# Performance work log

Hardware: AMD Instinct MI355X
Metric: run time of the kernel (lower is better)

The kernel has to match this reference:

```python
import jax, jax.numpy as jnp
import numpy as np

DIM = 1024
NUM_HEADS = 16
SEQ_LEN = 4096


def setup_inputs() -> dict:
    key = jax.random.key(0)
    ks = jax.random.split(key, 9)
    s = DIM ** -0.5  # typical init scale for weights
    return {
        "x": jax.random.normal(ks[0], (SEQ_LEN, DIM), dtype=jnp.float32),
        "Wq": jax.random.normal(ks[1], (DIM, DIM), dtype=jnp.float32) * s,
        "bq": jax.random.normal(ks[2], (DIM,), dtype=jnp.float32) * s,
        "Wk": jax.random.normal(ks[3], (DIM, DIM), dtype=jnp.float32) * s,
        "bk": jax.random.normal(ks[4], (DIM,), dtype=jnp.float32) * s,
        "Wv": jax.random.normal(ks[5], (DIM, DIM), dtype=jnp.float32) * s,
        "bv": jax.random.normal(ks[6], (DIM,), dtype=jnp.float32) * s,
        "Wp": jax.random.normal(ks[7], (DIM, DIM), dtype=jnp.float32) * s,
        "bp": jax.random.normal(ks[8], (DIM,), dtype=jnp.float32) * s,
    }


def reference(x, Wq, bq, Wk, bk, Wv, bv, Wp, bp):
    T, C = x.shape
    H = NUM_HEADS
    Dh = C // H
    # QKV projections (eqx.nn.Linear: y = W @ x + b, vmapped over tokens)
    q = (x @ Wq.T + bq).reshape(T, H, Dh).swapaxes(0, 1)  # [H, T, Dh]
    k = (x @ Wk.T + bk).reshape(T, H, Dh).swapaxes(0, 1)
    v = (x @ Wv.T + bv).reshape(T, H, Dh).swapaxes(0, 1)
    # NOTE: original scales by C**-0.5 (full dim), not head_dim**-0.5
    attn = jnp.einsum("htd,hsd->hts", q, k) * (C ** -0.5)  # [H, T, T]
    causal = jnp.tril(jnp.ones((T, T), dtype=bool))[None, :, :]
    attn = jnp.where(causal, attn, -jnp.inf)
    attn = jax.nn.softmax(attn, axis=-1)
    out = jnp.einsum("hts,hsd->htd", attn, v)  # [H, T, Dh]
    out = out.swapaxes(0, 1).reshape(T, C)
    return out @ Wp.T + bp
```

## Files before the change

### kernel.cpp

```cpp
#include <hip/hip_runtime.h>
#include <stdint.h>

typedef unsigned short u16;
typedef __bf16 bf16x8 __attribute__((ext_vector_type(8)));
typedef u16 u16x8 __attribute__((ext_vector_type(8)));
typedef u16 u16x4 __attribute__((ext_vector_type(4)));
typedef float f32x4 __attribute__((ext_vector_type(4)));
typedef float f32x16 __attribute__((ext_vector_type(16)));

#define SEQ 4096
#define CD 1024
#define NH 16
#define DHD 64

__device__ __forceinline__ u16 f2bf(float f) {
  union { float f; unsigned u; } v; v.f = f;
  unsigned r = v.u + 0x7fffu + ((v.u >> 16) & 1u);
  return (u16)(r >> 16);
}
__device__ __forceinline__ unsigned fbits(float f) {
  union { float f; unsigned u; } v; v.f = f; return v.u;
}

__device__ __forceinline__ void load_lds16(const u16* g, u16* l) {
  __builtin_amdgcn_global_load_lds((const __attribute__((address_space(1))) void*)g,
                                   (__attribute__((address_space(3))) void*)l, 16, 0, 0);
}

__global__ __launch_bounds__(256) void cvt_all(const float* __restrict__ x, const float* __restrict__ Wq,
                                               const float* __restrict__ Wk, const float* __restrict__ Wv,
                                               const float* __restrict__ Wp,
                                               u16* __restrict__ xb, u16* __restrict__ Wb, u16* __restrict__ Wpb) {
  int b = blockIdx.x;
  const float* src; u16* dst; int base;
  if (b < 2048)      { src = x;  dst = xb;             base = b; }
  else if (b < 2560) { src = Wq; dst = Wb;             base = b - 2048; }
  else if (b < 3072) { src = Wk; dst = Wb + CD * CD;   base = b - 2560; }
  else if (b < 3584) { src = Wv; dst = Wb + 2*CD*CD;   base = b - 3072; }
  else               { src = Wp; dst = Wpb;            base = b - 3584; }
  int i = (base * 256 + (int)threadIdx.x) * 8;
  float4 a = *(const float4*)(src + i);
  float4 c = *(const float4*)(src + i + 4);
  u16x8 o;
  o[0] = f2bf(a.x); o[1] = f2bf(a.y); o[2] = f2bf(a.z); o[3] = f2bf(a.w);
  o[4] = f2bf(c.x); o[5] = f2bf(c.y); o[6] = f2bf(c.z); o[7] = f2bf(c.w);
  *(u16x8*)(dst + i) = o;
}

template<int MODE>
__device__ __forceinline__ void gemm_core(const u16* __restrict__ A, const u16* __restrict__ Bw,
                                          const float* __restrict__ bias, void* __restrict__ outp,
                                          float oscale) {
  constexpr int K = CD, N = CD;
  __shared__ u16 As[128 * 32];
  __shared__ u16 Bs[128 * 32];
  const int tid = threadIdx.x;
  const int w = tid >> 6, L = tid & 63, q = L >> 4, ln = L & 15;
  const int rowA0 = blockIdx.y * 128, rowB0 = blockIdx.x * 128;
  const int wr = (w >> 1) * 64, wc = (w & 1) * 64;
  f32x4 acc[4][4] = {};
  for (int k0 = 0; k0 < K; k0 += 32) {
#pragma unroll
    for (int pass = 0; pass < 2; ++pass) {
      int off = pass * 4096 + tid * 16;
      int row = off >> 6;
      int cole = (off & 63) >> 1;
      load_lds16(A + (size_t)(rowA0 + row) * K + k0 + cole, As + pass * 2048 + w * 512);
      load_lds16(Bw + (size_t)(rowB0 + row) * K + k0 + cole, Bs + pass * 2048 + w * 512);
    }
    __syncthreads();
    bf16x8 af[4], bg[4];
#pragma unroll
    for (int i = 0; i < 4; ++i) af[i] = *(const bf16x8*)(As + (wr + i * 16 + ln) * 32 + q * 8);
#pragma unroll
    for (int i = 0; i < 4; ++i) bg[i] = *(const bf16x8*)(Bs + (wc + i * 16 + ln) * 32 + q * 8);
#pragma unroll
    for (int i = 0; i < 4; ++i)
#pragma unroll
      for (int j = 0; j < 4; ++j)
        acc[i][j] = __builtin_amdgcn_mfma_f32_16x16x32_bf16(af[i], bg[j], acc[i][j], 0, 0, 0);
    __syncthreads();
  }
#pragma unroll
  for (int i = 0; i < 4; ++i) {
#pragma unroll
    for (int j = 0; j < 4; ++j) {
      int col = rowB0 + wc + j * 16 + ln;
      float bb = bias[col];
#pragma unroll
      for (int r = 0; r < 4; ++r) {
        int row = rowA0 + wr + i * 16 + q * 4 + r;
        float v = (acc[i][j][r] + bb) * oscale;
        if (MODE == 0)      ((u16*)outp)[(size_t)row * N + col] = f2bf(v);
        else if (MODE == 1) ((u16*)outp)[(size_t)col * SEQ + row] = f2bf(v);
        else                ((float*)outp)[(size_t)row * N + col] = v;
      }
    }
  }
}

__global__ __launch_bounds__(256) void gemm_qkv(const u16* __restrict__ A, const u16* __restrict__ W3,
                                                const float* __restrict__ bq, const float* __restrict__ bk,
                                                const float* __restrict__ bv, u16* __restrict__ Qb,
                                                u16* __restrict__ Kb, u16* __restrict__ VTb) {
  int z = blockIdx.z;
  if (z == 0)      gemm_core<0>(A, W3,               bq, Qb,  0.03125f);
  else if (z == 1) gemm_core<0>(A, W3 + CD * CD,     bk, Kb,  1.0f);
  else             gemm_core<1>(A, W3 + 2 * CD * CD, bv, VTb, 1.0f);
}

__global__ __launch_bounds__(256) void gemm_proj(const u16* __restrict__ A, const u16* __restrict__ Bw,
                                                 const float* __restrict__ bias, float* __restrict__ out) {
  gemm_core<2>(A, Bw, bias, out, 1.0f);
}

__global__ __launch_bounds__(128) void attn_kernel(const u16* __restrict__ Q, const u16* __restrict__ Kg,
                                                   const u16* __restrict__ VTg, u16* __restrict__ O) {
  __shared__ u16 Ks[2][64 * 72];
  __shared__ u16 Vt[2][64 * 72];
  const int tid = threadIdx.x, w = tid >> 6, L = tid & 63;
  const int ln = L & 31, hh = L >> 5;
  const int b = blockIdx.x;
  const int qt = (SEQ / 64 - 1) - (b >> 4);
  const int h = b & 15;
  const int colH = h * DHD;
  const int qrow0 = qt * 64 + w * 32;
  bf16x8 qf[4];
#pragma unroll
  for (int kk = 0; kk < 4; ++kk)
    qf[kk] = *(const bf16x8*)(Q + (size_t)(qrow0 + ln) * CD + colH + kk * 16 + hh * 8);
  f32x16 oa[2] = {};
  float lsum = 0.f;
  const int srow = tid >> 3, sx = tid & 7;
  u16x8 kr[4], vr[4];
#pragma unroll
  for (int p = 0; p < 4; ++p) {
    kr[p] = *(const u16x8*)(Kg + (size_t)(p * 16 + srow) * CD + colH + sx * 8);
    vr[p] = *(const u16x8*)(VTg + (size_t)(colH + p * 16 + srow) * SEQ + sx * 8);
  }
  for (int jt = 0; jt <= qt; ++jt) {
    const int buf = jt & 1;
    u16* KsB = Ks[buf];
    u16* VtB = Vt[buf];
#pragma unroll
    for (int p = 0; p < 4; ++p) {
      *(u16x8*)(KsB + (p * 16 + srow) * 72 + sx * 8) = kr[p];
      *(u16x8*)(VtB + (p * 16 + srow) * 72 + sx * 8) = vr[p];
    }
    __syncthreads();
    if (jt < qt) {
      const size_t kb2 = (size_t)(jt + 1) * 64;
#pragma unroll
      for (int p = 0; p < 4; ++p) {
        kr[p] = *(const u16x8*)(Kg + (kb2 + p * 16 + srow) * CD + colH + sx * 8);
        vr[p] = *(const u16x8*)(VTg + (size_t)(colH + p * 16 + srow) * SEQ + kb2 + sx * 8);
      }
    }
    const bool diag = (jt == qt);
    unsigned pk[16];
#pragma unroll
    for (int nt = 0; nt < 2; ++nt) {
      f32x16 a = {};
#pragma unroll
      for (int kk = 0; kk < 4; ++kk) {
        bf16x8 kf = *(const bf16x8*)(KsB + (nt * 32 + ln) * 72 + kk * 16 + hh * 8);
        a = __builtin_amdgcn_mfma_f32_32x32x16_bf16(kf, qf[kk], a, 0, 0, 0);
      }
#pragma unroll
      for (int r = 0; r < 16; ++r) {
        float sv = a[r];
        if (diag) {
          const int key_l = nt * 32 + (r & 3) + 8 * (r >> 2) + 4 * hh;
          if (key_l > w * 32 + ln) sv = -1e30f;
        }
        float p = __expf(sv);
        lsum += p;
        a[r] = p;
      }
#pragma unroll
      for (int i = 0; i < 8; ++i)
        pk[nt * 8 + i] = __builtin_amdgcn_perm(fbits(a[2 * i + 1]), fbits(a[2 * i]), 0x07060302);
    }
#pragma unroll
    for (int b0 = 0; b0 < 16; b0 += 4) {
      asm("v_permlane32_swap_b32 %0, %1" : "+v"(pk[b0 + 0]), "+v"(pk[b0 + 2]));
      asm("v_permlane32_swap_b32 %0, %1" : "+v"(pk[b0 + 1]), "+v"(pk[b0 + 3]));
    }
#pragma unroll
    for (int g = 0; g < 2; ++g)
#pragma unroll
      for (int s = 0; s < 4; ++s) {
        bf16x8 vf = *(const bf16x8*)(VtB + (g * 32 + ln) * 72 + s * 16 + hh * 8);
        union { unsigned u[4]; bf16x8 v; } pf;
        pf.u[0] = pk[s * 4 + 0]; pf.u[1] = pk[s * 4 + 1];
        pf.u[2] = pk[s * 4 + 2]; pf.u[3] = pk[s * 4 + 3];
        oa[g] = __builtin_amdgcn_mfma_f32_32x32x16_bf16(vf, pf.v, oa[g], 0, 0, 0);
      }
  }
  lsum += __shfl_xor(lsum, 32, 64);
  const float inv = 1.0f / lsum;
#pragma unroll
  for (int g = 0; g < 2; ++g)
#pragma unroll
    for (int rg = 0; rg < 4; ++rg) {
      u16x4 ov;
#pragma unroll
      for (int i = 0; i < 4; ++i) ov[i] = f2bf(oa[g][rg * 4 + i] * inv);
      *(u16x4*)(O + (size_t)(qrow0 + ln) * CD + colH + g * 32 + 8 * rg + 4 * hh) = ov;
    }
}

extern "C" void kernel_launch(void* const* d_in, const int* in_sizes, int n_in,
                              void* d_out, int out_size, void* d_ws, size_t ws_size,
                              hipStream_t stream) {
  const float* x  = (const float*)d_in[0];
  const float* Wq = (const float*)d_in[1];
  const float* bq = (const float*)d_in[2];
  const float* Wk = (const float*)d_in[3];
  const float* bk = (const float*)d_in[4];
  const float* Wv = (const float*)d_in[5];
  const float* bv = (const float*)d_in[6];
  const float* Wp = (const float*)d_in[7];
  const float* bp = (const float*)d_in[8];

  char* ws = (char*)d_ws;
  u16* xb  = (u16*)(ws);
  u16* Wb  = (u16*)(ws + (8u << 20));
  u16* Wpb = (u16*)(ws + (14u << 20));
  u16* Qb  = (u16*)(ws + (16u << 20));
  u16* Kb  = (u16*)(ws + (24u << 20));
  u16* VTb = (u16*)(ws + (32u << 20));
  u16* Ab  = (u16*)(ws + (40u << 20));

  cvt_all<<<4096, 256, 0, stream>>>(x, Wq, Wk, Wv, Wp, xb, Wb, Wpb);
  gemm_qkv<<<dim3(CD / 128, SEQ / 128, 3), 256, 0, stream>>>(xb, Wb, bq, bk, bv, Qb, Kb, VTb);
  attn_kernel<<<(SEQ / 64) * NH, 128, 0, stream>>>(Qb, Kb, VTb, Ab);
  gemm_proj<<<dim3(CD / 128, SEQ / 128), 256, 0, stream>>>(Ab, Wpb, bp, (float*)d_out);
}
```

Baseline: 222.7 us.

## Double-buffer GEMM LDS tiles with register prefetch; split conversion kernel

Replaces the direct global-to-LDS loads in the shared GEMM core with register prefetch of the next K tile into a double-buffered LDS array. This drops one barrier per iteration and overlaps global loads with MFMA work. It also splits the single fused fp32-to-bf16 conversion kernel into five separate launches. The split adds launch overhead, and routing tiles through registers raises register pressure and adds LDS write instructions.

```diff
diff --git a/kernel.cpp b/kernel.cpp
--- a/kernel.cpp
+++ b/kernel.cpp
@@ -22,29 +22,15 @@
   union { float f; unsigned u; } v; v.f = f; return v.u;
 }
 
-__device__ __forceinline__ void load_lds16(const u16* g, u16* l) {
-  __builtin_amdgcn_global_load_lds((const __attribute__((address_space(1))) void*)g,
-                                   (__attribute__((address_space(3))) void*)l, 16, 0, 0);
-}
-
-__global__ __launch_bounds__(256) void cvt_all(const float* __restrict__ x, const float* __restrict__ Wq,
-                                               const float* __restrict__ Wk, const float* __restrict__ Wv,
-                                               const float* __restrict__ Wp,
-                                               u16* __restrict__ xb, u16* __restrict__ Wb, u16* __restrict__ Wpb) {
-  int b = blockIdx.x;
-  const float* src; u16* dst; int base;
-  if (b < 2048)      { src = x;  dst = xb;             base = b; }
-  else if (b < 2560) { src = Wq; dst = Wb;             base = b - 2048; }
-  else if (b < 3072) { src = Wk; dst = Wb + CD * CD;   base = b - 2560; }
-  else if (b < 3584) { src = Wv; dst = Wb + 2*CD*CD;   base = b - 3072; }
-  else               { src = Wp; dst = Wpb;            base = b - 3584; }
-  int i = (base * 256 + (int)threadIdx.x) * 8;
-  float4 a = *(const float4*)(src + i);
-  float4 c = *(const float4*)(src + i + 4);
+__global__ __launch_bounds__(256) void cvt_bf16(const float* __restrict__ in, u16* __restrict__ out, int n) {
+  int i = (blockIdx.x * 256 + threadIdx.x) * 8;
+  if (i >= n) return;
+  float4 a = *(const float4*)(in + i);
+  float4 b = *(const float4*)(in + i + 4);
   u16x8 o;
   o[0] = f2bf(a.x); o[1] = f2bf(a.y); o[2] = f2bf(a.z); o[3] = f2bf(a.w);
-  o[4] = f2bf(c.x); o[5] = f2bf(c.y); o[6] = f2bf(c.z); o[7] = f2bf(c.w);
-  *(u16x8*)(dst + i) = o;
+  o[4] = f2bf(b.x); o[5] = f2bf(b.y); o[6] = f2bf(b.z); o[7] = f2bf(b.w);
+  *(u16x8*)(out + i) = o;
 }
 
 template<int MODE>
@@ -52,34 +38,44 @@
                                           const float* __restrict__ bias, void* __restrict__ outp,
                                           float oscale) {
   constexpr int K = CD, N = CD;
-  __shared__ u16 As[128 * 32];
-  __shared__ u16 Bs[128 * 32];
+  __shared__ u16 As[2][128 * 32];
+  __shared__ u16 Bs[2][128 * 32];
   const int tid = threadIdx.x;
   const int w = tid >> 6, L = tid & 63, q = L >> 4, ln = L & 15;
   const int rowA0 = blockIdx.y * 128, rowB0 = blockIdx.x * 128;
   const int wr = (w >> 1) * 64, wc = (w & 1) * 64;
+  const int c0 = tid * 16, c1 = 4096 + tid * 16;
+  const int r0 = c0 >> 6, e0 = (c0 & 63) >> 1;
+  const int r1 = c1 >> 6, e1 = (c1 & 63) >> 1;
   f32x4 acc[4][4] = {};
+  u16x8 a0, a1, b0, b1;
+  a0 = *(const u16x8*)(A  + (size_t)(rowA0 + r0) * K + e0);
+  a1 = *(const u16x8*)(A  + (size_t)(rowA0 + r1) * K + e1);
+  b0 = *(const u16x8*)(Bw + (size_t)(rowB0 + r0) * K + e0);
+  b1 = *(const u16x8*)(Bw + (size_t)(rowB0 + r1) * K + e1);
   for (int k0 = 0; k0 < K; k0 += 32) {
-#pragma unroll
-    for (int pass = 0; pass < 2; ++pass) {
-      int off = pass * 4096 + tid * 16;
-      int row = off >> 6;
-      int cole = (off & 63) >> 1;
-      load_lds16(A + (size_t)(rowA0 + row) * K + k0 + cole, As + pass * 2048 + w * 512);
-      load_lds16(Bw + (size_t)(rowB0 + row) * K + k0 + cole, Bs + pass * 2048 + w * 512);
-    }
+    const int buf = (k0 >> 5) & 1;
+    *(u16x8*)(&As[buf][c0 >> 1]) = a0;
+    *(u16x8*)(&As[buf][c1 >> 1]) = a1;
+    *(u16x8*)(&Bs[buf][c0 >> 1]) = b0;
+    *(u16x8*)(&Bs[buf][c1 >> 1]) = b1;
     __syncthreads();
+    if (k0 + 32 < K) {
+      a0 = *(const u16x8*)(A  + (size_t)(rowA0 + r0) * K + k0 + 32 + e0);
+      a1 = *(const u16x8*)(A  + (size_t)(rowA0 + r1) * K + k0 + 32 + e1);
+      b0 = *(const u16x8*)(Bw + (size_t)(rowB0 + r0) * K + k0 + 32 + e0);
+      b1 = *(const u16x8*)(Bw + (size_t)(rowB0 + r1) * K + k0 + 32 + e1);
+    }
     bf16x8 af[4], bg[4];
 #pragma unroll
-    for (int i = 0; i < 4; ++i) af[i] = *(const bf16x8*)(As + (wr + i * 16 + ln) * 32 + q * 8);
-#pragma unroll
-    for (int i = 0; i < 4; ++i) bg[i] = *(const bf16x8*)(Bs + (wc + i * 16 + ln) * 32 + q * 8);
+    for (int i = 0; i < 4; ++i) af[i] = *(const bf16x8*)(&As[buf][(wr + i * 16 + ln) * 32 + q * 8]);
+#pragma unroll
+    for (int i = 0; i < 4; ++i) bg[i] = *(const bf16x8*)(&Bs[buf][(wc + i * 16 + ln) * 32 + q * 8]);
 #pragma unroll
     for (int i = 0; i < 4; ++i)
 #pragma unroll
       for (int j = 0; j < 4; ++j)
         acc[i][j] = __builtin_amdgcn_mfma_f32_16x16x32_bf16(af[i], bg[j], acc[i][j], 0, 0, 0);
-    __syncthreads();
   }
 #pragma unroll
   for (int i = 0; i < 4; ++i) {
@@ -232,7 +228,12 @@
   u16* VTb = (u16*)(ws + (32u << 20));
   u16* Ab  = (u16*)(ws + (40u << 20));
 
-  cvt_all<<<4096, 256, 0, stream>>>(x, Wq, Wk, Wv, Wp, xb, Wb, Wpb);
+  cvt_bf16<<<2048, 256, 0, stream>>>(x,  xb, SEQ * CD);
+  cvt_bf16<<<512, 256, 0, stream>>>(Wq, Wb,               CD * CD);
+  cvt_bf16<<<512, 256, 0, stream>>>(Wk, Wb + CD * CD,     CD * CD);
+  cvt_bf16<<<512, 256, 0, stream>>>(Wv, Wb + 2 * CD * CD, CD * CD);
+  cvt_bf16<<<512, 256, 0, stream>>>(Wp, Wpb,              CD * CD);
+
   gemm_qkv<<<dim3(CD / 128, SEQ / 128, 3), 256, 0, stream>>>(xb, Wb, bq, bk, bv, Qb, Kb, VTb);
   attn_kernel<<<(SEQ / 64) * NH, 128, 0, stream>>>(Qb, Kb, VTb, Ab);
   gemm_proj<<<dim3(CD / 128, SEQ / 128), 256, 0, stream>>>(Ab, Wpb, bp, (float*)d_out);
```

New measurement: 262.2 us. +17.8%, slower.
